# Optimization experiments

Hardware: AMD Instinct MI355X
Metric: run time of the kernel (lower is better)

## Reference

```python
import jax, jax.numpy as jnp
import numpy as np

HIDDEN = 32


def setup_inputs() -> dict:
    key = jax.random.key(0)
    ks = jax.random.split(key, 8)
    B, T, I = 1024, 512, 64
    s_ih = 1.0 / np.sqrt(HIDDEN)
    return {
        "x": jax.random.normal(ks[0], (B, T, I), dtype=jnp.float32),
        "h0": jnp.zeros((1, B, HIDDEN), dtype=jnp.float32),
        "W_ih": jax.random.uniform(ks[1], (HIDDEN, I), jnp.float32, -s_ih, s_ih),
        "b_ih": jax.random.uniform(ks[2], (HIDDEN,), jnp.float32, -s_ih, s_ih),
        "W_hh": jax.random.uniform(ks[3], (HIDDEN, HIDDEN), jnp.float32, -s_ih, s_ih),
        "b_hh": jax.random.uniform(ks[4], (HIDDEN,), jnp.float32, -s_ih, s_ih),
        "W_out": jax.random.uniform(ks[5], (1, HIDDEN), jnp.float32, -s_ih, s_ih),
        "b_out": jax.random.uniform(ks[6], (1,), jnp.float32, -s_ih, s_ih),
    }


def reference(x, h0, W_ih, b_ih, W_hh, b_hh, W_out, b_out):
    # x: [B, T, I]; h0: [1, B, H] (num_layers=1)
    # Precompute input contribution for all timesteps in one GEMM: [B, T, H]
    x_proj = jnp.einsum("bti,hi->bth", x, W_ih) + b_ih

    def step(h, xt):  # h: [B, H], xt: [B, H]
        h_new = jnp.tanh(xt + h @ W_hh.T + b_hh)
        return h_new, h_new

    h_last, r_out_t = jax.lax.scan(step, h0[0], jnp.swapaxes(x_proj, 0, 1))
    r_out = jnp.swapaxes(r_out_t, 0, 1)  # [B, T, H]
    # Per-timestep Linear(32 -> 1), batched as one GEMM: [B, T, 1]
    outs = r_out @ W_out.T + b_out
    return outs, h_last[None]
```

## Files before the change

kernel.cpp:

```cpp
#include <hip/hip_runtime.h>

#define Bc 1024
#define Tc 512
#define Ic 64
#define Hc 32
#define XP 516
#define LOG2E2 2.8853900817779268f

typedef __bf16 bf16x8 __attribute__((ext_vector_type(8)));
typedef __bf16 bf16x4 __attribute__((ext_vector_type(4)));
typedef float  f32x4  __attribute__((ext_vector_type(4)));
typedef _Float16 half2v __attribute__((ext_vector_type(2)));
typedef unsigned uint2v __attribute__((ext_vector_type(2)));

__device__ inline bf16x8 to_bf16x8(float4 u0, float4 u1) {
    bf16x8 t;
    t[0] = (__bf16)u0.x; t[1] = (__bf16)u0.y; t[2] = (__bf16)u0.z; t[3] = (__bf16)u0.w;
    t[4] = (__bf16)u1.x; t[5] = (__bf16)u1.y; t[6] = (__bf16)u1.z; t[7] = (__bf16)u1.w;
    return t;
}
__device__ inline bf16x8 to_bf16x8s(float4 u0, float4 u1, float s) {
    bf16x8 t;
    t[0] = (__bf16)(u0.x*s); t[1] = (__bf16)(u0.y*s); t[2] = (__bf16)(u0.z*s); t[3] = (__bf16)(u0.w*s);
    t[4] = (__bf16)(u1.x*s); t[5] = (__bf16)(u1.y*s); t[6] = (__bf16)(u1.z*s); t[7] = (__bf16)(u1.w*s);
    return t;
}


#if __has_builtin(__builtin_amdgcn_permlane16_swap)
#define PLSWAP(A, B)                                                          \
    { uint2v _t = __builtin_amdgcn_permlane16_swap((A), (B), false, false);   \
      (A) = _t[0]; (B) = _t[1]; }
#else
#define PLSWAP(A, B)                                                          \
    asm("s_nop 1\n\tv_permlane16_swap_b32 %0, %1" : "+v"(A), "+v"(B));
#endif

#define RORD(dst, src, N)                                                     \
    dst = (unsigned)__builtin_amdgcn_mov_dpp((int)(src), 0x120 + (N), 0xF, 0xF, false);

#if __has_builtin(__builtin_amdgcn_fdot2)
#define FDOT(g, W, a)                                                         \
    __builtin_amdgcn_fdot2(__builtin_bit_cast(half2v, (unsigned)(g)), (W), (a), false)
#else
__device__ inline float fdot2_emul(unsigned g, half2v w, float a) {
    half2v v = __builtin_bit_cast(half2v, g);
    a = fmaf((float)v[0], (float)w[0], a);
    return fmaf((float)v[1], (float)w[1], a);
}
#define FDOT(g, W, a) fdot2_emul((g), (W), (a))
#endif

#define GATHER(cc)                                                            \
    unsigned _r0 = (cc), _r1 = (cc);                                          \
    PLSWAP(_r0, _r1);                                                         \
    const unsigned _pt = psel ? _r0 : _r1;                                    \
    unsigned g0 = (_pt << 16) | ((cc) & 0xFFFFu);                             \
    unsigned g1, g2, g3, g4, g5, g6, g7, g8, g9, g10, g11, g12, g13, g14, g15;\
    RORD(g1, g0, 8)                                                           \
    RORD(g2, g0, 4)  RORD(g3, g1, 4)                                          \
    RORD(g4, g0, 2)  RORD(g5, g1, 2)  RORD(g6, g2, 2)  RORD(g7, g3, 2)        \
    RORD(g8, g0, 1)  RORD(g9, g1, 1)  RORD(g10, g2, 1) RORD(g11, g3, 1)       \
    RORD(g12, g4, 1) RORD(g13, g5, 1) RORD(g14, g6, 1) RORD(g15, g7, 1)

#define STEP(xval, uu)                                                        \
    {                                                                         \
        GATHER(c)                                                             \
        float a0 = (xval) + biasc, a1 = 0.f, a2 = 0.f, a3 = 0.f;              \
        a0 = FDOT(g0,  W0,  a0); a1 = FDOT(g1,  W1,  a1);                     \
        a2 = FDOT(g2,  W2,  a2); a3 = FDOT(g3,  W3,  a3);                     \
        a0 = FDOT(g4,  W4,  a0); a1 = FDOT(g5,  W5,  a1);                     \
        a2 = FDOT(g6,  W6,  a2); a3 = FDOT(g7,  W7,  a3);                     \
        a0 = FDOT(g8,  W8,  a0); a1 = FDOT(g9,  W9,  a1);                     \
        a2 = FDOT(g10, W10, a2); a3 = FDOT(g11, W11, a3);                     \
        a0 = FDOT(g12, W12, a0); a1 = FDOT(g13, W13, a1);                     \
        a2 = FDOT(g14, W14, a2); a3 = FDOT(g15, W15, a3);                     \
        const float a_ = (a0 + a1) + (a2 + a3);                               \
        const float p_ = __builtin_amdgcn_exp2f(a_);                          \
        rr = __builtin_amdgcn_rcpf(p_ + 1.0f);                                \
        const _Float16 rv_ = (_Float16)rr;                                    \
        c = (unsigned)__builtin_bit_cast(unsigned short, rv_);                \
        pbuf[half][uu][h] = fmaf(rr, w2o, wo);                                \
    }

#define CVT4(dst, src)                                                        \
    dst.x = (float)(src)[0]; dst.y = (float)(src)[1];                         \
    dst.z = (float)(src)[2]; dst.w = (float)(src)[3];

#define TILE_LOAD(Xn, bb, lt)                                                 \
    do {                                                                      \
        const float* xp_ =                                                    \
            x + ((size_t)(b0 + (bb)) * Tc + (lt) * 16 + m) * Ic + q * 8;      \
        Xn##0 = ((const float4*)xp_)[0];                                      \
        Xn##1 = ((const float4*)xp_)[1];                                      \
        Xn##2 = ((const float4*)(xp_ + 32))[0];                               \
        Xn##3 = ((const float4*)(xp_ + 32))[1];                               \
    } while (0)

#define TILE_MFMA(Xn, bb, lt)                                                 \
    do {                                                                      \
        const bf16x8 A0_ = to_bf16x8(Xn##0, Xn##1);                           \
        const bf16x8 A1_ = to_bf16x8(Xn##2, Xn##3);                           \
        f32x4 ac0 = {0.f, 0.f, 0.f, 0.f};                                     \
        f32x4 ac1 = {0.f, 0.f, 0.f, 0.f};                                     \
        ac0 = __builtin_amdgcn_mfma_f32_16x16x32_bf16(A0_, Bf[0][0], ac0, 0, 0, 0); \
        ac0 = __builtin_amdgcn_mfma_f32_16x16x32_bf16(A1_, Bf[0][1], ac0, 0, 0, 0); \
        ac1 = __builtin_amdgcn_mfma_f32_16x16x32_bf16(A0_, Bf[1][0], ac1, 0, 0, 0); \
        ac1 = __builtin_amdgcn_mfma_f32_16x16x32_bf16(A1_, Bf[1][1], ac1, 0, 0, 0); \
        bf16x4 p0_, p1_;                                                      \
        p0_[0] = (__bf16)(ac0[0] + bias0); p0_[1] = (__bf16)(ac0[1] + bias0); \
        p0_[2] = (__bf16)(ac0[2] + bias0); p0_[3] = (__bf16)(ac0[3] + bias0); \
        p1_[0] = (__bf16)(ac1[0] + bias1); p1_[1] = (__bf16)(ac1[1] + bias1); \
        p1_[2] = (__bf16)(ac1[2] + bias1); p1_[3] = (__bf16)(ac1[3] + bias1); \
        *(bf16x4*)&xq[bb][m][(lt) * 16 + q * 4]      = p0_;                   \
        *(bf16x4*)&xq[bb][m + 16][(lt) * 16 + q * 4] = p1_;                   \
    } while (0)

__global__ __launch_bounds__(64) void fused_rnn_kernel(
    const float* __restrict__ x, const float* __restrict__ Wih,
    const float* __restrict__ bih, const float* __restrict__ h0,
    const float* __restrict__ Whh, const float* __restrict__ bhh,
    const float* __restrict__ Wout, const float* __restrict__ bout,
    float* __restrict__ out)
{
    __shared__ __bf16   xq[2][Hc][XP];
    __shared__ float    pbuf[2][16][34];

    const int lane = threadIdx.x;
    const int half = lane >> 5;
    const int h    = lane & 31;
    const int m    = lane & 15;
    const int q    = lane >> 4;
    const int b0   = blockIdx.x * 2;

    bf16x8 Bf[2][2];
#pragma unroll
    for (int nh = 0; nh < 2; ++nh)
#pragma unroll
        for (int kh = 0; kh < 2; ++kh) {
            const float* wp = Wih + (m + 16 * nh) * Ic + q * 8 + kh * 32;
            Bf[nh][kh] = to_bf16x8s(((const float4*)wp)[0],
                                    ((const float4*)wp)[1], LOG2E2);
        }
    const float bias0 = bih[m] * LOG2E2;
    const float bias1 = bih[m + 16] * LOG2E2;

    unsigned ch = (unsigned)h;
    unsigned d0_ = ch, d1_ = ch;
    PLSWAP(d0_, d1_);
    const bool psel = ((d0_ & 0xFFFFu) == (unsigned)(h ^ 16));
    const unsigned part0 = psel ? d0_ : d1_;
    unsigned s0 = (part0 << 16) | ch;
    unsigned s1, s2, s3, s4, s5, s6, s7, s8, s9, s10, s11, s12, s13, s14, s15;
    RORD(s1, s0, 8)
    RORD(s2, s0, 4)  RORD(s3, s1, 4)
    RORD(s4, s0, 2)  RORD(s5, s1, 2)  RORD(s6, s2, 2)  RORD(s7, s3, 2)
    RORD(s8, s0, 1)  RORD(s9, s1, 1)  RORD(s10, s2, 1) RORD(s11, s3, 1)
    RORD(s12, s4, 1) RORD(s13, s5, 1) RORD(s14, s6, 1) RORD(s15, s7, 1)

    const float cw = -2.0f * LOG2E2;
    const float* wr = Whh + h * Hc;
#define MKW(Wk, sk)                                                           \
    half2v Wk;                                                                \
    {                                                                         \
        const unsigned il_ = (sk) & 0xFFFFu, ih_ = (sk) >> 16;                \
        Wk[0] = (_Float16)(wr[il_] * cw);                                     \
        Wk[1] = (_Float16)(wr[ih_] * cw);                                     \
    }
    MKW(W0, s0)   MKW(W1, s1)   MKW(W2, s2)   MKW(W3, s3)
    MKW(W4, s4)   MKW(W5, s5)   MKW(W6, s6)   MKW(W7, s7)
    MKW(W8, s8)   MKW(W9, s9)   MKW(W10, s10) MKW(W11, s11)
    MKW(W12, s12) MKW(W13, s13) MKW(W14, s14) MKW(W15, s15)
#undef MKW

    const float4* wrow = (const float4*)wr;
    const float4 t0 = wrow[0], t1 = wrow[1], t2 = wrow[2], t3 = wrow[3],
                 t4 = wrow[4], t5 = wrow[5], t6 = wrow[6], t7 = wrow[7];
    const float rsum =
        (((t0.x + t0.y) + (t0.z + t0.w)) + ((t1.x + t1.y) + (t1.z + t1.w))) +
        (((t2.x + t2.y) + (t2.z + t2.w)) + ((t3.x + t3.y) + (t3.z + t3.w))) +
        (((t4.x + t4.y) + (t4.z + t4.w)) + ((t5.x + t5.y) + (t5.z + t5.w))) +
        (((t6.x + t6.y) + (t6.z + t6.w)) + ((t7.x + t7.y) + (t7.z + t7.w)));
    const float biasc = (bhh[h] + rsum) * LOG2E2;
    const float wo  = Wout[h];
    const float w2o = -2.0f * wo;
    const float bo  = bout[0];

    float rr = fmaf(-0.5f, h0[(size_t)(b0 + half) * Hc + h], 0.5f);
    {
        const _Float16 rv0 = (_Float16)rr;
        ch = (unsigned)__builtin_bit_cast(unsigned short, rv0);
    }
    unsigned c = ch;
    float* orow = out + (size_t)(b0 + half) * Tc;

    float4 Xa0, Xa1, Xa2, Xa3, Xb0, Xb1, Xb2, Xb3;
    TILE_LOAD(Xa, 0, 0);  TILE_LOAD(Xb, 1, 0);
    TILE_MFMA(Xa, 0, 0);  TILE_MFMA(Xb, 1, 0);
    TILE_LOAD(Xa, 0, 1);  TILE_LOAD(Xb, 1, 1);
    TILE_MFMA(Xa, 0, 1);  TILE_MFMA(Xb, 1, 1);
    TILE_LOAD(Xa, 0, 2);  TILE_LOAD(Xb, 1, 2);
    __syncthreads();

    const __bf16* xrow = &xq[half][h][0];

    bf16x4 r0 = *(const bf16x4*)(xrow + 0), r1 = *(const bf16x4*)(xrow + 4),
           r2 = *(const bf16x4*)(xrow + 8), r3 = *(const bf16x4*)(xrow + 12);
    float4 q0, q1, q2, q3;
    CVT4(q0, r0) CVT4(q1, r1) CVT4(q2, r2) CVT4(q3, r3)

#pragma unroll 1
    for (int tb = 0; tb < Tc / 16; ++tb) {
        const int tbn = (tb + 1 < Tc / 16) ? tb + 1 : tb;
        const __bf16* nx = xrow + tbn * 16;
        const bf16x4 m0 = *(const bf16x4*)(nx + 0),
                     m1 = *(const bf16x4*)(nx + 4),
                     m2 = *(const bf16x4*)(nx + 8),
                     m3 = *(const bf16x4*)(nx + 12);

        if (tb + 2 < Tc / 16) { TILE_MFMA(Xa, 0, tb + 2); TILE_MFMA(Xb, 1, tb + 2); }
        if (tb + 3 < Tc / 16) { TILE_LOAD(Xa, 0, tb + 3); TILE_LOAD(Xb, 1, tb + 3); }

        STEP(q0.x, 0)  STEP(q0.y, 1)  STEP(q0.z, 2)  STEP(q0.w, 3)
        STEP(q1.x, 4)  STEP(q1.y, 5)  STEP(q1.z, 6)  STEP(q1.w, 7)
        STEP(q2.x, 8)  STEP(q2.y, 9)  STEP(q2.z, 10) STEP(q2.w, 11)
        STEP(q3.x, 12) STEP(q3.y, 13) STEP(q3.z, 14) STEP(q3.w, 15)

        __builtin_amdgcn_wave_barrier();

        if (h < 16) {
            const float2* pr = (const float2*)pbuf[half][h];
            float2 sa = pr[0], sb = pr[1];
#pragma unroll
            for (int mm = 2; mm < 16; mm += 2) {
                sa.x += pr[mm].x;     sa.y += pr[mm].y;
                sb.x += pr[mm + 1].x; sb.y += pr[mm + 1].y;
            }
            orow[tb * 16 + h] = ((sa.x + sb.x) + (sa.y + sb.y)) + bo;
        }
        __builtin_amdgcn_wave_barrier();

        CVT4(q0, m0) CVT4(q1, m1) CVT4(q2, m2) CVT4(q3, m3)
    }

    out[(size_t)Bc * Tc + (size_t)(b0 + half) * Hc + h] = fmaf(-2.0f, rr, 1.0f);
}

extern "C" void kernel_launch(void* const* d_in, const int* in_sizes, int n_in,
                              void* d_out, int out_size, void* d_ws, size_t ws_size,
                              hipStream_t stream) {
    const float* x    = (const float*)d_in[0];
    const float* h0   = (const float*)d_in[1];
    const float* Wih  = (const float*)d_in[2];
    const float* bih  = (const float*)d_in[3];
    const float* Whh  = (const float*)d_in[4];
    const float* bhh  = (const float*)d_in[5];
    const float* Wout = (const float*)d_in[6];
    const float* bout = (const float*)d_in[7];
    float* out = (float*)d_out;

    fused_rnn_kernel<<<Bc / 2, 64, 0, stream>>>(x, Wih, bih, h0, Whh, bhh,
                                                Wout, bout, out);
}
```

Baseline: 229.1 us.

## Pack four batch rows per wave with two hidden units per lane

Each 64-lane wave now handles four batch rows instead of two. Each lane owns two hidden units packed as a half2, so the recurrent gather needs only 16-lane row rotations via DPP and no permlane16 swap. The input projection buffer shrinks to a double-buffered small ring in LDS, and the output reduction is reorganised around the new layout. The grid halves, which may lower occupancy and latency hiding across CUs, while each wave does twice the FDOT work per step.

```diff
diff --git a/kernel.cpp b/kernel.cpp
--- a/kernel.cpp
+++ b/kernel.cpp
@@ -4,14 +4,16 @@
 #define Tc 512
 #define Ic 64
 #define Hc 32
-#define XP 516
 #define LOG2E2 2.8853900817779268f
+
+#define XT_ROW 24
+#define XT_BAT (Hc * XT_ROW)
+#define XT_BUF (4 * XT_BAT)
 
 typedef __bf16 bf16x8 __attribute__((ext_vector_type(8)));
 typedef __bf16 bf16x4 __attribute__((ext_vector_type(4)));
 typedef float  f32x4  __attribute__((ext_vector_type(4)));
 typedef _Float16 half2v __attribute__((ext_vector_type(2)));
-typedef unsigned uint2v __attribute__((ext_vector_type(2)));
 
 __device__ inline bf16x8 to_bf16x8(float4 u0, float4 u1) {
     bf16x8 t;
@@ -26,15 +28,6 @@
     return t;
 }
 
-
-#if __has_builtin(__builtin_amdgcn_permlane16_swap)
-#define PLSWAP(A, B)                                                          \
-    { uint2v _t = __builtin_amdgcn_permlane16_swap((A), (B), false, false);   \
-      (A) = _t[0]; (B) = _t[1]; }
-#else
-#define PLSWAP(A, B)                                                          \
-    asm("s_nop 1\n\tv_permlane16_swap_b32 %0, %1" : "+v"(A), "+v"(B));
-#endif
 
 #define RORD(dst, src, N)                                                     \
     dst = (unsigned)__builtin_amdgcn_mov_dpp((int)(src), 0x120 + (N), 0xF, 0xF, false);
@@ -51,53 +44,58 @@
 #define FDOT(g, W, a) fdot2_emul((g), (W), (a))
 #endif
 
-#define GATHER(cc)                                                            \
-    unsigned _r0 = (cc), _r1 = (cc);                                          \
-    PLSWAP(_r0, _r1);                                                         \
-    const unsigned _pt = psel ? _r0 : _r1;                                    \
-    unsigned g0 = (_pt << 16) | ((cc) & 0xFFFFu);                             \
-    unsigned g1, g2, g3, g4, g5, g6, g7, g8, g9, g10, g11, g12, g13, g14, g15;\
-    RORD(g1, g0, 8)                                                           \
-    RORD(g2, g0, 4)  RORD(g3, g1, 4)                                          \
-    RORD(g4, g0, 2)  RORD(g5, g1, 2)  RORD(g6, g2, 2)  RORD(g7, g3, 2)        \
-    RORD(g8, g0, 1)  RORD(g9, g1, 1)  RORD(g10, g2, 1) RORD(g11, g3, 1)       \
-    RORD(g12, g4, 1) RORD(g13, g5, 1) RORD(g14, g6, 1) RORD(g15, g7, 1)
-
-#define STEP(xval, uu)                                                        \
+#define STEP(xv0, xv1, uu)                                                    \
     {                                                                         \
-        GATHER(c)                                                             \
-        float a0 = (xval) + biasc, a1 = 0.f, a2 = 0.f, a3 = 0.f;              \
-        a0 = FDOT(g0,  W0,  a0); a1 = FDOT(g1,  W1,  a1);                     \
-        a2 = FDOT(g2,  W2,  a2); a3 = FDOT(g3,  W3,  a3);                     \
-        a0 = FDOT(g4,  W4,  a0); a1 = FDOT(g5,  W5,  a1);                     \
-        a2 = FDOT(g6,  W6,  a2); a3 = FDOT(g7,  W7,  a3);                     \
-        a0 = FDOT(g8,  W8,  a0); a1 = FDOT(g9,  W9,  a1);                     \
-        a2 = FDOT(g10, W10, a2); a3 = FDOT(g11, W11, a3);                     \
-        a0 = FDOT(g12, W12, a0); a1 = FDOT(g13, W13, a1);                     \
-        a2 = FDOT(g14, W14, a2); a3 = FDOT(g15, W15, a3);                     \
-        const float a_ = (a0 + a1) + (a2 + a3);                               \
-        const float p_ = __builtin_amdgcn_exp2f(a_);                          \
-        rr = __builtin_amdgcn_rcpf(p_ + 1.0f);                                \
-        const _Float16 rv_ = (_Float16)rr;                                    \
-        c = (unsigned)__builtin_bit_cast(unsigned short, rv_);                \
-        pbuf[half][uu][h] = fmaf(rr, w2o, wo);                                \
-    }
-
-#define CVT4(dst, src)                                                        \
-    dst.x = (float)(src)[0]; dst.y = (float)(src)[1];                         \
-    dst.z = (float)(src)[2]; dst.w = (float)(src)[3];
+        unsigned g1, g2, g3, g4, g5, g6, g7, g8, g9, g10, g11, g12, g13, g14, g15; \
+        RORD(g1, c, 1)   RORD(g2, c, 2)   RORD(g3, c, 3)   RORD(g4, c, 4)     \
+        RORD(g5, c, 5)   RORD(g6, c, 6)   RORD(g7, c, 7)   RORD(g8, c, 8)     \
+        RORD(g9, c, 9)   RORD(g10, c, 10) RORD(g11, c, 11) RORD(g12, c, 12)   \
+        RORD(g13, c, 13) RORD(g14, c, 14) RORD(g15, c, 15)                    \
+        float a00 = (xv0) + biasc0, a01 = 0.f, a02 = 0.f, a03 = 0.f;          \
+        float a10 = (xv1) + biasc1, a11 = 0.f, a12 = 0.f, a13 = 0.f;          \
+        a00 = FDOT(c,   W0_0,  a00);  a10 = FDOT(c,   W1_0,  a10);            \
+        a01 = FDOT(g1,  W0_1,  a01);  a11 = FDOT(g1,  W1_1,  a11);            \
+        a02 = FDOT(g2,  W0_2,  a02);  a12 = FDOT(g2,  W1_2,  a12);            \
+        a03 = FDOT(g3,  W0_3,  a03);  a13 = FDOT(g3,  W1_3,  a13);            \
+        a00 = FDOT(g4,  W0_4,  a00);  a10 = FDOT(g4,  W1_4,  a10);            \
+        a01 = FDOT(g5,  W0_5,  a01);  a11 = FDOT(g5,  W1_5,  a11);            \
+        a02 = FDOT(g6,  W0_6,  a02);  a12 = FDOT(g6,  W1_6,  a12);            \
+        a03 = FDOT(g7,  W0_7,  a03);  a13 = FDOT(g7,  W1_7,  a13);            \
+        a00 = FDOT(g8,  W0_8,  a00);  a10 = FDOT(g8,  W1_8,  a10);            \
+        a01 = FDOT(g9,  W0_9,  a01);  a11 = FDOT(g9,  W1_9,  a11);            \
+        a02 = FDOT(g10, W0_10, a02);  a12 = FDOT(g10, W1_10, a12);            \
+        a03 = FDOT(g11, W0_11, a03);  a13 = FDOT(g11, W1_11, a13);            \
+        a00 = FDOT(g12, W0_12, a00);  a10 = FDOT(g12, W1_12, a10);            \
+        a01 = FDOT(g13, W0_13, a01);  a11 = FDOT(g13, W1_13, a11);            \
+        a02 = FDOT(g14, W0_14, a02);  a12 = FDOT(g14, W1_14, a12);            \
+        a03 = FDOT(g15, W0_15, a03);  a13 = FDOT(g15, W1_15, a13);            \
+        const float A0 = (a00 + a01) + (a02 + a03);                           \
+        const float A1 = (a10 + a11) + (a12 + a13);                           \
+        const float p0_ = __builtin_amdgcn_exp2f(A0);                         \
+        const float p1_ = __builtin_amdgcn_exp2f(A1);                         \
+        rr0 = __builtin_amdgcn_rcpf(p0_ + 1.0f);                              \
+        rr1 = __builtin_amdgcn_rcpf(p1_ + 1.0f);                              \
+        c = __builtin_bit_cast(unsigned, __builtin_amdgcn_cvt_pkrtz(rr0, rr1)); \
+        pbuf[uu][g][m2] = fmaf(rr0, w2o0, fmaf(rr1, w2o1, wos));              \
+    }
+
+#define CVT8(dlo, dhi, src)                                                   \
+    dlo.x = (float)(src)[0]; dlo.y = (float)(src)[1];                         \
+    dlo.z = (float)(src)[2]; dlo.w = (float)(src)[3];                         \
+    dhi.x = (float)(src)[4]; dhi.y = (float)(src)[5];                         \
+    dhi.z = (float)(src)[6]; dhi.w = (float)(src)[7];
 
 #define TILE_LOAD(Xn, bb, lt)                                                 \
     do {                                                                      \
         const float* xp_ =                                                    \
-            x + ((size_t)(b0 + (bb)) * Tc + (lt) * 16 + m) * Ic + q * 8;      \
+            x + ((size_t)(b0 + (bb)) * Tc + (lt) * 16 + m2) * Ic + q * 8;     \
         Xn##0 = ((const float4*)xp_)[0];                                      \
         Xn##1 = ((const float4*)xp_)[1];                                      \
         Xn##2 = ((const float4*)(xp_ + 32))[0];                               \
         Xn##3 = ((const float4*)(xp_ + 32))[1];                               \
     } while (0)
 
-#define TILE_MFMA(Xn, bb, lt)                                                 \
+#define TILE_MFMA(Xn, tp)                                                     \
     do {                                                                      \
         const bf16x8 A0_ = to_bf16x8(Xn##0, Xn##1);                           \
         const bf16x8 A1_ = to_bf16x8(Xn##2, Xn##3);                           \
@@ -112,138 +110,157 @@
         p0_[2] = (__bf16)(ac0[2] + bias0); p0_[3] = (__bf16)(ac0[3] + bias0); \
         p1_[0] = (__bf16)(ac1[0] + bias1); p1_[1] = (__bf16)(ac1[1] + bias1); \
         p1_[2] = (__bf16)(ac1[2] + bias1); p1_[3] = (__bf16)(ac1[3] + bias1); \
-        *(bf16x4*)&xq[bb][m][(lt) * 16 + q * 4]      = p0_;                   \
-        *(bf16x4*)&xq[bb][m + 16][(lt) * 16 + q * 4] = p1_;                   \
+        *(bf16x4*)&(tp)[m2 * XT_ROW + q * 4]        = p0_;                    \
+        *(bf16x4*)&(tp)[(m2 + 16) * XT_ROW + q * 4] = p1_;                    \
     } while (0)
 
-__global__ __launch_bounds__(64) void fused_rnn_kernel(
+__global__ __launch_bounds__(64, 1) void fused_rnn_kernel(
     const float* __restrict__ x, const float* __restrict__ Wih,
     const float* __restrict__ bih, const float* __restrict__ h0,
     const float* __restrict__ Whh, const float* __restrict__ bhh,
     const float* __restrict__ Wout, const float* __restrict__ bout,
     float* __restrict__ out)
 {
-    __shared__ __bf16   xq[2][Hc][XP];
-    __shared__ float    pbuf[2][16][34];
+    __shared__ __bf16 xt[2 * XT_BUF];
+    __shared__ float  pbuf[16][4][20];
 
     const int lane = threadIdx.x;
-    const int half = lane >> 5;
-    const int h    = lane & 31;
-    const int m    = lane & 15;
+    const int m2   = lane & 15;
     const int q    = lane >> 4;
-    const int b0   = blockIdx.x * 2;
+    const int g    = q;
+    const int b0   = blockIdx.x * 4;
+    const int hh0  = 2 * m2, hh1 = 2 * m2 + 1;
 
     bf16x8 Bf[2][2];
 #pragma unroll
     for (int nh = 0; nh < 2; ++nh)
 #pragma unroll
         for (int kh = 0; kh < 2; ++kh) {
-            const float* wp = Wih + (m + 16 * nh) * Ic + q * 8 + kh * 32;
+            const float* wp = Wih + (m2 + 16 * nh) * Ic + q * 8 + kh * 32;
             Bf[nh][kh] = to_bf16x8s(((const float4*)wp)[0],
                                     ((const float4*)wp)[1], LOG2E2);
         }
-    const float bias0 = bih[m] * LOG2E2;
-    const float bias1 = bih[m + 16] * LOG2E2;
-
-    unsigned ch = (unsigned)h;
-    unsigned d0_ = ch, d1_ = ch;
-    PLSWAP(d0_, d1_);
-    const bool psel = ((d0_ & 0xFFFFu) == (unsigned)(h ^ 16));
-    const unsigned part0 = psel ? d0_ : d1_;
-    unsigned s0 = (part0 << 16) | ch;
+    const float bias0 = bih[m2] * LOG2E2;
+    const float bias1 = bih[m2 + 16] * LOG2E2;
+
+    unsigned s0 = (unsigned)hh0 | ((unsigned)hh1 << 16);
     unsigned s1, s2, s3, s4, s5, s6, s7, s8, s9, s10, s11, s12, s13, s14, s15;
-    RORD(s1, s0, 8)
-    RORD(s2, s0, 4)  RORD(s3, s1, 4)
-    RORD(s4, s0, 2)  RORD(s5, s1, 2)  RORD(s6, s2, 2)  RORD(s7, s3, 2)
-    RORD(s8, s0, 1)  RORD(s9, s1, 1)  RORD(s10, s2, 1) RORD(s11, s3, 1)
-    RORD(s12, s4, 1) RORD(s13, s5, 1) RORD(s14, s6, 1) RORD(s15, s7, 1)
+    RORD(s1, s0, 1)   RORD(s2, s0, 2)   RORD(s3, s0, 3)   RORD(s4, s0, 4)
+    RORD(s5, s0, 5)   RORD(s6, s0, 6)   RORD(s7, s0, 7)   RORD(s8, s0, 8)
+    RORD(s9, s0, 9)   RORD(s10, s0, 10) RORD(s11, s0, 11) RORD(s12, s0, 12)
+    RORD(s13, s0, 13) RORD(s14, s0, 14) RORD(s15, s0, 15)
 
     const float cw = -2.0f * LOG2E2;
-    const float* wr = Whh + h * Hc;
-#define MKW(Wk, sk)                                                           \
-    half2v Wk;                                                                \
+    const float* wr0 = Whh + hh0 * Hc;
+    const float* wr1 = Whh + hh1 * Hc;
+#define MKW2(W0k, W1k, sk)                                                    \
+    half2v W0k, W1k;                                                          \
     {                                                                         \
-        const unsigned il_ = (sk) & 0xFFFFu, ih_ = (sk) >> 16;                \
-        Wk[0] = (_Float16)(wr[il_] * cw);                                     \
-        Wk[1] = (_Float16)(wr[ih_] * cw);                                     \
-    }
-    MKW(W0, s0)   MKW(W1, s1)   MKW(W2, s2)   MKW(W3, s3)
-    MKW(W4, s4)   MKW(W5, s5)   MKW(W6, s6)   MKW(W7, s7)
-    MKW(W8, s8)   MKW(W9, s9)   MKW(W10, s10) MKW(W11, s11)
-    MKW(W12, s12) MKW(W13, s13) MKW(W14, s14) MKW(W15, s15)
-#undef MKW
-
-    const float4* wrow = (const float4*)wr;
-    const float4 t0 = wrow[0], t1 = wrow[1], t2 = wrow[2], t3 = wrow[3],
-                 t4 = wrow[4], t5 = wrow[5], t6 = wrow[6], t7 = wrow[7];
-    const float rsum =
-        (((t0.x + t0.y) + (t0.z + t0.w)) + ((t1.x + t1.y) + (t1.z + t1.w))) +
-        (((t2.x + t2.y) + (t2.z + t2.w)) + ((t3.x + t3.y) + (t3.z + t3.w))) +
-        (((t4.x + t4.y) + (t4.z + t4.w)) + ((t5.x + t5.y) + (t5.z + t5.w))) +
-        (((t6.x + t6.y) + (t6.z + t6.w)) + ((t7.x + t7.y) + (t7.z + t7.w)));
-    const float biasc = (bhh[h] + rsum) * LOG2E2;
-    const float wo  = Wout[h];
-    const float w2o = -2.0f * wo;
-    const float bo  = bout[0];
-
-    float rr = fmaf(-0.5f, h0[(size_t)(b0 + half) * Hc + h], 0.5f);
+        const unsigned jl_ = (sk) & 0xFFFFu, jh_ = (sk) >> 16;                \
+        W0k[0] = (_Float16)(wr0[jl_] * cw); W0k[1] = (_Float16)(wr0[jh_] * cw); \
+        W1k[0] = (_Float16)(wr1[jl_] * cw); W1k[1] = (_Float16)(wr1[jh_] * cw); \
+    }
+    MKW2(W0_0,  W1_0,  s0)   MKW2(W0_1,  W1_1,  s1)
+    MKW2(W0_2,  W1_2,  s2)   MKW2(W0_3,  W1_3,  s3)
+    MKW2(W0_4,  W1_4,  s4)   MKW2(W0_5,  W1_5,  s5)
+    MKW2(W0_6,  W1_6,  s6)   MKW2(W0_7,  W1_7,  s7)
+    MKW2(W0_8,  W1_8,  s8)   MKW2(W0_9,  W1_9,  s9)
+    MKW2(W0_10, W1_10, s10)  MKW2(W0_11, W1_11, s11)
+    MKW2(W0_12, W1_12, s12)  MKW2(W0_13, W1_13, s13)
+    MKW2(W0_14, W1_14, s14)  MKW2(W0_15, W1_15, s15)
+#undef MKW2
+
+    float rs0 = 0.f, rs1 = 0.f;
+#pragma unroll
+    for (int j = 0; j < Hc; ++j) { rs0 += wr0[j]; rs1 += wr1[j]; }
+    const float biasc0 = (bhh[hh0] + rs0) * LOG2E2;
+    const float biasc1 = (bhh[hh1] + rs1) * LOG2E2;
+    const float wo0 = Wout[hh0], wo1 = Wout[hh1];
+    const float w2o0 = -2.0f * wo0, w2o1 = -2.0f * wo1;
+    const float wos  = wo0 + wo1;
+    const float bo   = bout[0];
+
+    float rr0 = fmaf(-0.5f, h0[(size_t)(b0 + g) * Hc + hh0], 0.5f);
+    float rr1 = fmaf(-0.5f, h0[(size_t)(b0 + g) * Hc + hh1], 0.5f);
+    unsigned c = __builtin_bit_cast(unsigned, __builtin_amdgcn_cvt_pkrtz(rr0, rr1));
+    float* orow = out + (size_t)(b0 + g) * Tc;
+
+    float4 Xa0, Xa1, Xa2, Xa3, Xb0, Xb1, Xb2, Xb3,
+           Xc0, Xc1, Xc2, Xc3, Xd0, Xd1, Xd2, Xd3;
+    TILE_LOAD(Xa, 0, 0); TILE_LOAD(Xb, 1, 0); TILE_LOAD(Xc, 2, 0); TILE_LOAD(Xd, 3, 0);
     {
-        const _Float16 rv0 = (_Float16)rr;
-        ch = (unsigned)__builtin_bit_cast(unsigned short, rv0);
-    }
-    unsigned c = ch;
-    float* orow = out + (size_t)(b0 + half) * Tc;
-
-    float4 Xa0, Xa1, Xa2, Xa3, Xb0, Xb1, Xb2, Xb3;
-    TILE_LOAD(Xa, 0, 0);  TILE_LOAD(Xb, 1, 0);
-    TILE_MFMA(Xa, 0, 0);  TILE_MFMA(Xb, 1, 0);
-    TILE_LOAD(Xa, 0, 1);  TILE_LOAD(Xb, 1, 1);
-    TILE_MFMA(Xa, 0, 1);  TILE_MFMA(Xb, 1, 1);
-    TILE_LOAD(Xa, 0, 2);  TILE_LOAD(Xb, 1, 2);
+        __bf16* tp = xt;
+        TILE_MFMA(Xa, tp + 0 * XT_BAT); TILE_MFMA(Xb, tp + 1 * XT_BAT);
+        TILE_MFMA(Xc, tp + 2 * XT_BAT); TILE_MFMA(Xd, tp + 3 * XT_BAT);
+    }
+    TILE_LOAD(Xa, 0, 1); TILE_LOAD(Xb, 1, 1); TILE_LOAD(Xc, 2, 1); TILE_LOAD(Xd, 3, 1);
+    {
+        __bf16* tp = xt + XT_BUF;
+        TILE_MFMA(Xa, tp + 0 * XT_BAT); TILE_MFMA(Xb, tp + 1 * XT_BAT);
+        TILE_MFMA(Xc, tp + 2 * XT_BAT); TILE_MFMA(Xd, tp + 3 * XT_BAT);
+    }
+    TILE_LOAD(Xa, 0, 2); TILE_LOAD(Xb, 1, 2); TILE_LOAD(Xc, 2, 2); TILE_LOAD(Xd, 3, 2);
     __syncthreads();
 
-    const __bf16* xrow = &xq[half][h][0];
-
-    bf16x4 r0 = *(const bf16x4*)(xrow + 0), r1 = *(const bf16x4*)(xrow + 4),
-           r2 = *(const bf16x4*)(xrow + 8), r3 = *(const bf16x4*)(xrow + 12);
-    float4 q0, q1, q2, q3;
-    CVT4(q0, r0) CVT4(q1, r1) CVT4(q2, r2) CVT4(q3, r3)
+    const __bf16* xr0base = xt + g * XT_BAT + hh0 * XT_ROW;
+    const __bf16* xr1base = xt + g * XT_BAT + hh1 * XT_ROW;
+
+    bf16x8 na0 = *(const bf16x8*)(xr0base), na1 = *(const bf16x8*)(xr0base + 8);
+    bf16x8 nb0 = *(const bf16x8*)(xr1base), nb1 = *(const bf16x8*)(xr1base + 8);
+    float4 qa0, qa1, qa2, qa3, qb0, qb1, qb2, qb3;
+    CVT8(qa0, qa1, na0) CVT8(qa2, qa3, na1)
+    CVT8(qb0, qb1, nb0) CVT8(qb2, qb3, nb1)
 
 #pragma unroll 1
     for (int tb = 0; tb < Tc / 16; ++tb) {
         const int tbn = (tb + 1 < Tc / 16) ? tb + 1 : tb;
-        const __bf16* nx = xrow + tbn * 16;
-        const bf16x4 m0 = *(const bf16x4*)(nx + 0),
-                     m1 = *(const bf16x4*)(nx + 4),
-                     m2 = *(const bf16x4*)(nx + 8),
-                     m3 = *(const bf16x4*)(nx + 12);
-
-        if (tb + 2 < Tc / 16) { TILE_MFMA(Xa, 0, tb + 2); TILE_MFMA(Xb, 1, tb + 2); }
-        if (tb + 3 < Tc / 16) { TILE_LOAD(Xa, 0, tb + 3); TILE_LOAD(Xb, 1, tb + 3); }
-
-        STEP(q0.x, 0)  STEP(q0.y, 1)  STEP(q0.z, 2)  STEP(q0.w, 3)
-        STEP(q1.x, 4)  STEP(q1.y, 5)  STEP(q1.z, 6)  STEP(q1.w, 7)
-        STEP(q2.x, 8)  STEP(q2.y, 9)  STEP(q2.z, 10) STEP(q2.w, 11)
-        STEP(q3.x, 12) STEP(q3.y, 13) STEP(q3.z, 14) STEP(q3.w, 15)
+        const __bf16* xr0 = xr0base + (tbn & 1) * XT_BUF;
+        const __bf16* xr1 = xr1base + (tbn & 1) * XT_BUF;
+        na0 = *(const bf16x8*)(xr0); na1 = *(const bf16x8*)(xr0 + 8);
+        nb0 = *(const bf16x8*)(xr1); nb1 = *(const bf16x8*)(xr1 + 8);
+
+        if (tb + 2 < Tc / 16) {
+            __bf16* tp = xt + (tb & 1) * XT_BUF;
+            TILE_MFMA(Xa, tp + 0 * XT_BAT); TILE_MFMA(Xb, tp + 1 * XT_BAT);
+            TILE_MFMA(Xc, tp + 2 * XT_BAT); TILE_MFMA(Xd, tp + 3 * XT_BAT);
+        }
+        if (tb + 3 < Tc / 16) {
+            TILE_LOAD(Xa, 0, tb + 3); TILE_LOAD(Xb, 1, tb + 3);
+            TILE_LOAD(Xc, 2, tb + 3); TILE_LOAD(Xd, 3, tb + 3);
+        }
+
+        STEP(qa0.x, qb0.x, 0)  STEP(qa0.y, qb0.y, 1)
+        STEP(qa0.z, qb0.z, 2)  STEP(qa0.w, qb0.w, 3)
+        STEP(qa1.x, qb1.x, 4)  STEP(qa1.y, qb1.y, 5)
+        STEP(qa1.z, qb1.z, 6)  STEP(qa1.w, qb1.w, 7)
+        STEP(qa2.x, qb2.x, 8)  STEP(qa2.y, qb2.y, 9)
+        STEP(qa2.z, qb2.z, 10) STEP(qa2.w, qb2.w, 11)
+        STEP(qa3.x, qb3.x, 12) STEP(qa3.y, qb3.y, 13)
+        STEP(qa3.z, qb3.z, 14) STEP(qa3.w, qb3.w, 15)
 
         __builtin_amdgcn_wave_barrier();
 
-        if (h < 16) {
-            const float2* pr = (const float2*)pbuf[half][h];
-            float2 sa = pr[0], sb = pr[1];
-#pragma unroll
-            for (int mm = 2; mm < 16; mm += 2) {
-                sa.x += pr[mm].x;     sa.y += pr[mm].y;
-                sb.x += pr[mm + 1].x; sb.y += pr[mm + 1].y;
-            }
-            orow[tb * 16 + h] = ((sa.x + sb.x) + (sa.y + sb.y)) + bo;
+        {
+            const float4* pr = (const float4*)&pbuf[m2][g][0];
+            const float4 s0_ = pr[0], s1_ = pr[1], s2_ = pr[2], s3_ = pr[3];
+            const float s =
+                (((s0_.x + s0_.y) + (s0_.z + s0_.w)) +
+                 ((s1_.x + s1_.y) + (s1_.z + s1_.w))) +
+                (((s2_.x + s2_.y) + (s2_.z + s2_.w)) +
+                 ((s3_.x + s3_.y) + (s3_.z + s3_.w)));
+            orow[tb * 16 + m2] = s + bo;
         }
         __builtin_amdgcn_wave_barrier();
 
-        CVT4(q0, m0) CVT4(q1, m1) CVT4(q2, m2) CVT4(q3, m3)
-    }
-
-    out[(size_t)Bc * Tc + (size_t)(b0 + half) * Hc + h] = fmaf(-2.0f, rr, 1.0f);
+        CVT8(qa0, qa1, na0) CVT8(qa2, qa3, na1)
+        CVT8(qb0, qb1, nb0) CVT8(qb2, qb3, nb1)
+    }
+
+    float2* hl = (float2*)(out + (size_t)Bc * Tc + (size_t)(b0 + g) * Hc + hh0);
+    float2 hv;
+    hv.x = fmaf(-2.0f, rr0, 1.0f);
+    hv.y = fmaf(-2.0f, rr1, 1.0f);
+    *hl = hv;
 }
 
 extern "C" void kernel_launch(void* const* d_in, const int* in_sizes, int n_in,
@@ -259,6 +276,6 @@
     const float* bout = (const float*)d_in[7];
     float* out = (float*)d_out;
 
-    fused_rnn_kernel<<<Bc / 2, 64, 0, stream>>>(x, Wih, bih, h0, Whh, bhh,
+    fused_rnn_kernel<<<Bc / 4, 64, 0, stream>>>(x, Wih, bih, h0, Whh, bhh,
                                                 Wout, bout, out);
 }
```

After: 249.3 us. +8.8%, slower.

## Split each hidden state across full wave: one batch per block with K-split matvec

Applied to the files above, without the earlier changes.

Each 64-lane block now handles one batch row instead of two. Each hidden unit's recurrent dot product is split across the two wave halves (8 fdot2 per half) and the halves are combined with permlane32_swap. The hidden state is repacked as even/odd fp16 pairs using permlane16_swap and cvt_pkrtz. The input projection is staged through a small double-buffered LDS tile instead of a whole-sequence buffer, and the grid doubles to 1024 blocks. This shortens the per-step serial dependency chain and adds occupancy, at the cost of extra cross-lane swaps per step and twice as many blocks each streaming x.

```diff
diff --git a/kernel.cpp b/kernel.cpp
--- a/kernel.cpp
+++ b/kernel.cpp
@@ -4,8 +4,10 @@
 #define Tc 512
 #define Ic 64
 #define Hc 32
-#define XP 516
-#define LOG2E2 2.8853900817779268f
+#define L2E2 2.8853900817779268f
+
+#define XT_ROW 24
+#define XT_BUF (Hc * XT_ROW)
 
 typedef __bf16 bf16x8 __attribute__((ext_vector_type(8)));
 typedef __bf16 bf16x4 __attribute__((ext_vector_type(4)));
@@ -26,6 +28,9 @@
     return t;
 }
 
+
+#define RORD(dst, src, N)                                                     \
+    dst = (unsigned)__builtin_amdgcn_mov_dpp((int)(src), 0x120 + (N), 0xF, 0xF, false);
 
 #if __has_builtin(__builtin_amdgcn_permlane16_swap)
 #define PLSWAP(A, B)                                                          \
@@ -36,8 +41,14 @@
     asm("s_nop 1\n\tv_permlane16_swap_b32 %0, %1" : "+v"(A), "+v"(B));
 #endif
 
-#define RORD(dst, src, N)                                                     \
-    dst = (unsigned)__builtin_amdgcn_mov_dpp((int)(src), 0x120 + (N), 0xF, 0xF, false);
+#if __has_builtin(__builtin_amdgcn_permlane32_swap)
+#define P32SWAP(A, B)                                                         \
+    { uint2v _t = __builtin_amdgcn_permlane32_swap((A), (B), false, false);   \
+      (A) = _t[0]; (B) = _t[1]; }
+#else
+#define P32SWAP(A, B)                                                         \
+    asm("s_nop 1\n\tv_permlane32_swap_b32 %0, %1" : "+v"(A), "+v"(B));
+#endif
 
 #if __has_builtin(__builtin_amdgcn_fdot2)
 #define FDOT(g, W, a)                                                         \
@@ -51,56 +62,54 @@
 #define FDOT(g, W, a) fdot2_emul((g), (W), (a))
 #endif
 
-#define GATHER(cc)                                                            \
-    unsigned _r0 = (cc), _r1 = (cc);                                          \
-    PLSWAP(_r0, _r1);                                                         \
-    const unsigned _pt = psel ? _r0 : _r1;                                    \
-    unsigned g0 = (_pt << 16) | ((cc) & 0xFFFFu);                             \
-    unsigned g1, g2, g3, g4, g5, g6, g7, g8, g9, g10, g11, g12, g13, g14, g15;\
-    RORD(g1, g0, 8)                                                           \
-    RORD(g2, g0, 4)  RORD(g3, g1, 4)                                          \
-    RORD(g4, g0, 2)  RORD(g5, g1, 2)  RORD(g6, g2, 2)  RORD(g7, g3, 2)        \
-    RORD(g8, g0, 1)  RORD(g9, g1, 1)  RORD(g10, g2, 1) RORD(g11, g3, 1)       \
-    RORD(g12, g4, 1) RORD(g13, g5, 1) RORD(g14, g6, 1) RORD(g15, g7, 1)
-
-#define STEP(xval, uu)                                                        \
+#define STEP(xv, uu)                                                          \
     {                                                                         \
-        GATHER(c)                                                             \
-        float a0 = (xval) + biasc, a1 = 0.f, a2 = 0.f, a3 = 0.f;              \
-        a0 = FDOT(g0,  W0,  a0); a1 = FDOT(g1,  W1,  a1);                     \
-        a2 = FDOT(g2,  W2,  a2); a3 = FDOT(g3,  W3,  a3);                     \
-        a0 = FDOT(g4,  W4,  a0); a1 = FDOT(g5,  W5,  a1);                     \
-        a2 = FDOT(g6,  W6,  a2); a3 = FDOT(g7,  W7,  a3);                     \
-        a0 = FDOT(g8,  W8,  a0); a1 = FDOT(g9,  W9,  a1);                     \
-        a2 = FDOT(g10, W10, a2); a3 = FDOT(g11, W11, a3);                     \
-        a0 = FDOT(g12, W12, a0); a1 = FDOT(g13, W13, a1);                     \
-        a2 = FDOT(g14, W14, a2); a3 = FDOT(g15, W15, a3);                     \
-        const float a_ = (a0 + a1) + (a2 + a3);                               \
-        const float p_ = __builtin_amdgcn_exp2f(a_);                          \
+        unsigned c8;                                                          \
+        RORD(c8, c, 8)                                                        \
+        const unsigned bse = rlo ? c : c8;                                    \
+        unsigned g1, g2, g3, g4, g5, g6, g7;                                  \
+        RORD(g1, bse, 1) RORD(g2, bse, 2) RORD(g3, bse, 3) RORD(g4, bse, 4)   \
+        RORD(g5, bse, 5) RORD(g6, bse, 6) RORD(g7, bse, 7)                    \
+        float a0 = FDOT(bse, W0, (xv));                                       \
+        float a1 = FDOT(g1,  W1, bch);                                        \
+        a0 = FDOT(g2, W2, a0);  a1 = FDOT(g3, W3, a1);                        \
+        a0 = FDOT(g4, W4, a0);  a1 = FDOT(g5, W5, a1);                        \
+        a0 = FDOT(g6, W6, a0);  a1 = FDOT(g7, W7, a1);                        \
+        const float Ah = a0 + a1;                                             \
+        unsigned sa = __builtin_bit_cast(unsigned, Ah), sb2 = sa;             \
+        P32SWAP(sa, sb2)                                                      \
+        const float A = __builtin_bit_cast(float, sa) +                       \
+                        __builtin_bit_cast(float, sb2);                       \
+        const float p_ = __builtin_amdgcn_exp2f(A);                           \
         rr = __builtin_amdgcn_rcpf(p_ + 1.0f);                                \
-        const _Float16 rv_ = (_Float16)rr;                                    \
-        c = (unsigned)__builtin_bit_cast(unsigned short, rv_);                \
-        pbuf[half][uu][h] = fmaf(rr, w2o, wo);                                \
-    }
-
-#define CVT4(dst, src)                                                        \
-    dst.x = (float)(src)[0]; dst.y = (float)(src)[1];                         \
-    dst.z = (float)(src)[2]; dst.w = (float)(src)[3];
-
-#define TILE_LOAD(Xn, bb, lt)                                                 \
+        pbuf[uu][hh] = fmaf(rr, w2o, wo);                                     \
+        unsigned P0 = __builtin_bit_cast(unsigned, rr), P1 = P0;              \
+        PLSWAP(P0, P1)                                                        \
+        const float rrp = __builtin_bit_cast(float, psel ? P0 : P1);          \
+        const float ev = rodd ? rrp : rr;                                     \
+        const float od = rodd ? rr : rrp;                                     \
+        c = __builtin_bit_cast(unsigned, __builtin_amdgcn_cvt_pkrtz(ev, od)); \
+    }
+
+#define CVT8(dlo, dhi, src)                                                   \
+    dlo.x = (float)(src)[0]; dlo.y = (float)(src)[1];                         \
+    dlo.z = (float)(src)[2]; dlo.w = (float)(src)[3];                         \
+    dhi.x = (float)(src)[4]; dhi.y = (float)(src)[5];                         \
+    dhi.z = (float)(src)[6]; dhi.w = (float)(src)[7];
+
+#define TILE_LOAD(lt)                                                         \
     do {                                                                      \
-        const float* xp_ =                                                    \
-            x + ((size_t)(b0 + (bb)) * Tc + (lt) * 16 + m) * Ic + q * 8;      \
-        Xn##0 = ((const float4*)xp_)[0];                                      \
-        Xn##1 = ((const float4*)xp_)[1];                                      \
-        Xn##2 = ((const float4*)(xp_ + 32))[0];                               \
-        Xn##3 = ((const float4*)(xp_ + 32))[1];                               \
+        const float* xp_ = x + ((size_t)b * Tc + (lt) * 16 + m2) * Ic + r * 8;\
+        Xa0 = ((const float4*)xp_)[0];                                        \
+        Xa1 = ((const float4*)xp_)[1];                                        \
+        Xa2 = ((const float4*)(xp_ + 32))[0];                                 \
+        Xa3 = ((const float4*)(xp_ + 32))[1];                                 \
     } while (0)
 
-#define TILE_MFMA(Xn, bb, lt)                                                 \
+#define TILE_MFMA(tp)                                                         \
     do {                                                                      \
-        const bf16x8 A0_ = to_bf16x8(Xn##0, Xn##1);                           \
-        const bf16x8 A1_ = to_bf16x8(Xn##2, Xn##3);                           \
+        const bf16x8 A0_ = to_bf16x8(Xa0, Xa1);                               \
+        const bf16x8 A1_ = to_bf16x8(Xa2, Xa3);                               \
         f32x4 ac0 = {0.f, 0.f, 0.f, 0.f};                                     \
         f32x4 ac1 = {0.f, 0.f, 0.f, 0.f};                                     \
         ac0 = __builtin_amdgcn_mfma_f32_16x16x32_bf16(A0_, Bf[0][0], ac0, 0, 0, 0); \
@@ -112,138 +121,136 @@
         p0_[2] = (__bf16)(ac0[2] + bias0); p0_[3] = (__bf16)(ac0[3] + bias0); \
         p1_[0] = (__bf16)(ac1[0] + bias1); p1_[1] = (__bf16)(ac1[1] + bias1); \
         p1_[2] = (__bf16)(ac1[2] + bias1); p1_[3] = (__bf16)(ac1[3] + bias1); \
-        *(bf16x4*)&xq[bb][m][(lt) * 16 + q * 4]      = p0_;                   \
-        *(bf16x4*)&xq[bb][m + 16][(lt) * 16 + q * 4] = p1_;                   \
+        *(bf16x4*)&(tp)[m2 * XT_ROW + r * 4]        = p0_;                    \
+        *(bf16x4*)&(tp)[(m2 + 16) * XT_ROW + r * 4] = p1_;                    \
     } while (0)
 
-__global__ __launch_bounds__(64) void fused_rnn_kernel(
+__global__ __launch_bounds__(64, 1) void fused_rnn_kernel(
     const float* __restrict__ x, const float* __restrict__ Wih,
     const float* __restrict__ bih, const float* __restrict__ h0,
     const float* __restrict__ Whh, const float* __restrict__ bhh,
     const float* __restrict__ Wout, const float* __restrict__ bout,
     float* __restrict__ out)
 {
-    __shared__ __bf16   xq[2][Hc][XP];
-    __shared__ float    pbuf[2][16][34];
+    __shared__ __bf16 xt[2 * XT_BUF];
+    __shared__ float  pbuf[16][36];
 
     const int lane = threadIdx.x;
-    const int half = lane >> 5;
-    const int h    = lane & 31;
-    const int m    = lane & 15;
-    const int q    = lane >> 4;
-    const int b0   = blockIdx.x * 2;
-
+    const int m2   = lane & 15;
+    const int r    = lane >> 4;
+    const bool rlo  = (lane < 32);
+    const bool rodd = (r & 1);
+    const int  hh   = 2 * m2 + (r & 1);
+    const int  b    = blockIdx.x;
+
+    const float shalf = 0.5f * L2E2;
     bf16x8 Bf[2][2];
 #pragma unroll
     for (int nh = 0; nh < 2; ++nh)
 #pragma unroll
         for (int kh = 0; kh < 2; ++kh) {
-            const float* wp = Wih + (m + 16 * nh) * Ic + q * 8 + kh * 32;
+            const float* wp = Wih + (m2 + 16 * nh) * Ic + r * 8 + kh * 32;
             Bf[nh][kh] = to_bf16x8s(((const float4*)wp)[0],
-                                    ((const float4*)wp)[1], LOG2E2);
+                                    ((const float4*)wp)[1], shalf);
         }
-    const float bias0 = bih[m] * LOG2E2;
-    const float bias1 = bih[m + 16] * LOG2E2;
-
-    unsigned ch = (unsigned)h;
-    unsigned d0_ = ch, d1_ = ch;
-    PLSWAP(d0_, d1_);
-    const bool psel = ((d0_ & 0xFFFFu) == (unsigned)(h ^ 16));
-    const unsigned part0 = psel ? d0_ : d1_;
-    unsigned s0 = (part0 << 16) | ch;
-    unsigned s1, s2, s3, s4, s5, s6, s7, s8, s9, s10, s11, s12, s13, s14, s15;
-    RORD(s1, s0, 8)
-    RORD(s2, s0, 4)  RORD(s3, s1, 4)
-    RORD(s4, s0, 2)  RORD(s5, s1, 2)  RORD(s6, s2, 2)  RORD(s7, s3, 2)
-    RORD(s8, s0, 1)  RORD(s9, s1, 1)  RORD(s10, s2, 1) RORD(s11, s3, 1)
-    RORD(s12, s4, 1) RORD(s13, s5, 1) RORD(s14, s6, 1) RORD(s15, s7, 1)
-
-    const float cw = -2.0f * LOG2E2;
-    const float* wr = Whh + h * Hc;
+    const float bias0 = bih[m2] * shalf;
+    const float bias1 = bih[m2 + 16] * shalf;
+
+    bool psel;
+    {
+        unsigned d0 = (unsigned)lane, d1 = (unsigned)lane;
+        PLSWAP(d0, d1)
+        psel = (d0 == (unsigned)(lane ^ 16));
+    }
+
+    unsigned s0p = (unsigned)(2 * m2) | ((unsigned)(2 * m2 + 1) << 16);
+    unsigned s8p;
+    RORD(s8p, s0p, 8)
+    const unsigned sbp = rlo ? s0p : s8p;
+    unsigned sk1, sk2, sk3, sk4, sk5, sk6, sk7;
+    RORD(sk1, sbp, 1) RORD(sk2, sbp, 2) RORD(sk3, sbp, 3) RORD(sk4, sbp, 4)
+    RORD(sk5, sbp, 5) RORD(sk6, sbp, 6) RORD(sk7, sbp, 7)
+
+    const float cw = -2.0f * L2E2;
+    const float* wrh = Whh + hh * Hc;
 #define MKW(Wk, sk)                                                           \
     half2v Wk;                                                                \
     {                                                                         \
-        const unsigned il_ = (sk) & 0xFFFFu, ih_ = (sk) >> 16;                \
-        Wk[0] = (_Float16)(wr[il_] * cw);                                     \
-        Wk[1] = (_Float16)(wr[ih_] * cw);                                     \
-    }
-    MKW(W0, s0)   MKW(W1, s1)   MKW(W2, s2)   MKW(W3, s3)
-    MKW(W4, s4)   MKW(W5, s5)   MKW(W6, s6)   MKW(W7, s7)
-    MKW(W8, s8)   MKW(W9, s9)   MKW(W10, s10) MKW(W11, s11)
-    MKW(W12, s12) MKW(W13, s13) MKW(W14, s14) MKW(W15, s15)
+        const unsigned jl_ = (sk) & 0xFFFFu, jh_ = (sk) >> 16;                \
+        Wk[0] = (_Float16)(wrh[jl_] * cw);                                    \
+        Wk[1] = (_Float16)(wrh[jh_] * cw);                                    \
+    }
+    MKW(W0, sbp) MKW(W1, sk1) MKW(W2, sk2) MKW(W3, sk3)
+    MKW(W4, sk4) MKW(W5, sk5) MKW(W6, sk6) MKW(W7, sk7)
 #undef MKW
 
-    const float4* wrow = (const float4*)wr;
-    const float4 t0 = wrow[0], t1 = wrow[1], t2 = wrow[2], t3 = wrow[3],
-                 t4 = wrow[4], t5 = wrow[5], t6 = wrow[6], t7 = wrow[7];
-    const float rsum =
-        (((t0.x + t0.y) + (t0.z + t0.w)) + ((t1.x + t1.y) + (t1.z + t1.w))) +
-        (((t2.x + t2.y) + (t2.z + t2.w)) + ((t3.x + t3.y) + (t3.z + t3.w))) +
-        (((t4.x + t4.y) + (t4.z + t4.w)) + ((t5.x + t5.y) + (t5.z + t5.w))) +
-        (((t6.x + t6.y) + (t6.z + t6.w)) + ((t7.x + t7.y) + (t7.z + t7.w)));
-    const float biasc = (bhh[h] + rsum) * LOG2E2;
-    const float wo  = Wout[h];
+    float rs = 0.f;
+#pragma unroll
+    for (int j = 0; j < Hc; ++j) rs += wrh[j];
+    const float bch = (bhh[hh] + rs) * shalf;
+    const float wo  = Wout[hh];
     const float w2o = -2.0f * wo;
     const float bo  = bout[0];
 
-    float rr = fmaf(-0.5f, h0[(size_t)(b0 + half) * Hc + h], 0.5f);
-    {
-        const _Float16 rv0 = (_Float16)rr;
-        ch = (unsigned)__builtin_bit_cast(unsigned short, rv0);
-    }
-    unsigned c = ch;
-    float* orow = out + (size_t)(b0 + half) * Tc;
-
-    float4 Xa0, Xa1, Xa2, Xa3, Xb0, Xb1, Xb2, Xb3;
-    TILE_LOAD(Xa, 0, 0);  TILE_LOAD(Xb, 1, 0);
-    TILE_MFMA(Xa, 0, 0);  TILE_MFMA(Xb, 1, 0);
-    TILE_LOAD(Xa, 0, 1);  TILE_LOAD(Xb, 1, 1);
-    TILE_MFMA(Xa, 0, 1);  TILE_MFMA(Xb, 1, 1);
-    TILE_LOAD(Xa, 0, 2);  TILE_LOAD(Xb, 1, 2);
+    const float h0e = h0[(size_t)b * Hc + 2 * m2];
+    const float h0o = h0[(size_t)b * Hc + 2 * m2 + 1];
+    const float re0 = fmaf(-0.5f, h0e, 0.5f);
+    const float ro0 = fmaf(-0.5f, h0o, 0.5f);
+    unsigned c = __builtin_bit_cast(unsigned, __builtin_amdgcn_cvt_pkrtz(re0, ro0));
+    float rr = rodd ? ro0 : re0;
+    float* orow = out + (size_t)b * Tc;
+
+    float4 Xa0, Xa1, Xa2, Xa3;
+    TILE_LOAD(0);
+    TILE_MFMA(xt);
+    TILE_LOAD(1);
+    TILE_MFMA(xt + XT_BUF);
+    TILE_LOAD(2);
     __syncthreads();
 
-    const __bf16* xrow = &xq[half][h][0];
-
-    bf16x4 r0 = *(const bf16x4*)(xrow + 0), r1 = *(const bf16x4*)(xrow + 4),
-           r2 = *(const bf16x4*)(xrow + 8), r3 = *(const bf16x4*)(xrow + 12);
-    float4 q0, q1, q2, q3;
-    CVT4(q0, r0) CVT4(q1, r1) CVT4(q2, r2) CVT4(q3, r3)
+    const __bf16* xrbase = xt + hh * XT_ROW;
+
+    bf16x8 na0 = *(const bf16x8*)(xrbase), na1 = *(const bf16x8*)(xrbase + 8);
+    float4 qa0, qa1, qa2, qa3;
+    CVT8(qa0, qa1, na0) CVT8(qa2, qa3, na1)
 
 #pragma unroll 1
     for (int tb = 0; tb < Tc / 16; ++tb) {
         const int tbn = (tb + 1 < Tc / 16) ? tb + 1 : tb;
-        const __bf16* nx = xrow + tbn * 16;
-        const bf16x4 m0 = *(const bf16x4*)(nx + 0),
-                     m1 = *(const bf16x4*)(nx + 4),
-                     m2 = *(const bf16x4*)(nx + 8),
-                     m3 = *(const bf16x4*)(nx + 12);
-
-        if (tb + 2 < Tc / 16) { TILE_MFMA(Xa, 0, tb + 2); TILE_MFMA(Xb, 1, tb + 2); }
-        if (tb + 3 < Tc / 16) { TILE_LOAD(Xa, 0, tb + 3); TILE_LOAD(Xb, 1, tb + 3); }
-
-        STEP(q0.x, 0)  STEP(q0.y, 1)  STEP(q0.z, 2)  STEP(q0.w, 3)
-        STEP(q1.x, 4)  STEP(q1.y, 5)  STEP(q1.z, 6)  STEP(q1.w, 7)
-        STEP(q2.x, 8)  STEP(q2.y, 9)  STEP(q2.z, 10) STEP(q2.w, 11)
-        STEP(q3.x, 12) STEP(q3.y, 13) STEP(q3.z, 14) STEP(q3.w, 15)
+        const __bf16* xr = xrbase + (tbn & 1) * XT_BUF;
+        na0 = *(const bf16x8*)(xr); na1 = *(const bf16x8*)(xr + 8);
+
+        if (tb + 2 < Tc / 16) { TILE_MFMA(xt + (tb & 1) * XT_BUF); }
+        if (tb + 3 < Tc / 16) { TILE_LOAD(tb + 3); }
+
+        STEP(qa0.x, 0)  STEP(qa0.y, 1)  STEP(qa0.z, 2)  STEP(qa0.w, 3)
+        STEP(qa1.x, 4)  STEP(qa1.y, 5)  STEP(qa1.z, 6)  STEP(qa1.w, 7)
+        STEP(qa2.x, 8)  STEP(qa2.y, 9)  STEP(qa2.z, 10) STEP(qa2.w, 11)
+        STEP(qa3.x, 12) STEP(qa3.y, 13) STEP(qa3.z, 14) STEP(qa3.w, 15)
 
         __builtin_amdgcn_wave_barrier();
 
-        if (h < 16) {
-            const float2* pr = (const float2*)pbuf[half][h];
-            float2 sa = pr[0], sb = pr[1];
-#pragma unroll
-            for (int mm = 2; mm < 16; mm += 2) {
-                sa.x += pr[mm].x;     sa.y += pr[mm].y;
-                sb.x += pr[mm + 1].x; sb.y += pr[mm + 1].y;
-            }
-            orow[tb * 16 + h] = ((sa.x + sb.x) + (sa.y + sb.y)) + bo;
+        if (lane < 16) {
+            const float4* pr = (const float4*)&pbuf[lane][0];
+            const float4 s0_ = pr[0], s1_ = pr[1], s2_ = pr[2], s3_ = pr[3];
+            const float4 s4_ = pr[4], s5_ = pr[5], s6_ = pr[6], s7_ = pr[7];
+            const float s =
+                ((((s0_.x + s0_.y) + (s0_.z + s0_.w)) +
+                  ((s1_.x + s1_.y) + (s1_.z + s1_.w))) +
+                 (((s2_.x + s2_.y) + (s2_.z + s2_.w)) +
+                  ((s3_.x + s3_.y) + (s3_.z + s3_.w)))) +
+                ((((s4_.x + s4_.y) + (s4_.z + s4_.w)) +
+                  ((s5_.x + s5_.y) + (s5_.z + s5_.w))) +
+                 (((s6_.x + s6_.y) + (s6_.z + s6_.w)) +
+                  ((s7_.x + s7_.y) + (s7_.z + s7_.w))));
+            orow[tb * 16 + lane] = s + bo;
         }
         __builtin_amdgcn_wave_barrier();
 
-        CVT4(q0, m0) CVT4(q1, m1) CVT4(q2, m2) CVT4(q3, m3)
-    }
-
-    out[(size_t)Bc * Tc + (size_t)(b0 + half) * Hc + h] = fmaf(-2.0f, rr, 1.0f);
+        CVT8(qa0, qa1, na0) CVT8(qa2, qa3, na1)
+    }
+
+    out[(size_t)Bc * Tc + (size_t)b * Hc + hh] = fmaf(-2.0f, rr, 1.0f);
 }
 
 extern "C" void kernel_launch(void* const* d_in, const int* in_sizes, int n_in,
@@ -259,6 +266,6 @@
     const float* bout = (const float*)d_in[7];
     float* out = (float*)d_out;
 
-    fused_rnn_kernel<<<Bc / 2, 64, 0, stream>>>(x, Wih, bih, h0, Whh, bhh,
-                                                Wout, bout, out);
-}
+    fused_rnn_kernel<<<Bc, 64, 0, stream>>>(x, Wih, bih, h0, Whh, bhh,
+                                            Wout, bout, out);
+}
```

Measured after the change: 225.2 us. No clear change (-1.7%).
